# Kernel optimization log

Measured on AMD Instinct MI355X. Metric: run time of the kernel, lower is better.

Reference implementation:

```python
import jax, jax.numpy as jnp
import numpy as np


def _make_coord(n):
    # grid-center coords in (-1, 1), matching make_coord in the torch code
    return -1.0 + 1.0 / n + (2.0 / n) * jnp.arange(n, dtype=jnp.float32)


def _mlp(inp, W1, b1, W2, b2, W3, b3):
    h = jax.nn.relu(inp @ W1 + b1)
    h = jax.nn.relu(h @ W2 + b2)
    return h @ W3 + b3


def setup_inputs() -> dict:
    key = jax.random.key(0)
    ks = jax.random.split(key, 4)
    dim = 64
    x = jax.random.normal(ks[0], (4, dim, 64, 64), dtype=jnp.float32)
    W1 = jax.random.normal(ks[1], (dim + 2, 256), dtype=jnp.float32) * 0.05
    W2 = jax.random.normal(ks[2], (256, 256), dtype=jnp.float32) * 0.05
    W3 = jax.random.normal(ks[3], (256, dim), dtype=jnp.float32) * 0.05
    return {
        "x": x,
        "W1": W1, "b1": jnp.zeros((256,), jnp.float32),
        "W2": W2, "b2": jnp.zeros((256,), jnp.float32),
        "W3": W3, "b3": jnp.zeros((dim,), jnp.float32),
        "h_out": 256, "w_out": 256,
    }


def reference(x, W1, b1, W2, b2, W3, b3, h_out, w_out):
    B, C, H, W = x.shape
    # query coords on the output grid (same for every batch element)
    gy, gx = jnp.meshgrid(_make_coord(h_out), _make_coord(w_out), indexing="ij")
    cy = gy.reshape(-1)  # [Q], coord channel 0 (height)
    cx = gx.reshape(-1)  # [Q], coord channel 1 (width)
    rx = 1.0 / H  # = 2 / H / 2
    ry = 1.0 / W
    eps_shift = 1e-6
    lim = 1.0 - 1e-6
    fy = _make_coord(H)  # feat_coord values along height
    fx = _make_coord(W)

    preds = []
    areas = []
    for vx in (-1.0, 1.0):
        for vy in (-1.0, 1.0):
            sy = jnp.clip(cy + vx * rx + eps_shift, -lim, lim)
            sx = jnp.clip(cx + vy * ry + eps_shift, -lim, lim)
            # grid_sample nearest, align_corners=False: unnormalize then round
            iy = jnp.clip(jnp.round(((sy + 1.0) * H - 1.0) * 0.5), 0, H - 1).astype(jnp.int32)
            ix = jnp.clip(jnp.round(((sx + 1.0) * W - 1.0) * 0.5), 0, W - 1).astype(jnp.int32)
            q_feat = x[:, :, iy, ix].transpose(0, 2, 1)  # [B, Q, C]
            rel_y = (cy - fy[iy]) * H  # [Q]
            rel_x = (cx - fx[ix]) * W
            rel = jnp.stack([rel_y, rel_x], axis=-1)  # [Q, 2]
            inp = jnp.concatenate(
                [q_feat, jnp.broadcast_to(rel, (B,) + rel.shape)], axis=-1
            )  # [B, Q, C+2]
            preds.append(_mlp(inp, W1, b1, W2, b2, W3, b3))  # [B, Q, C]
            areas.append(jnp.abs(rel_y * rel_x) + 1e-9)  # [Q]

    tot_area = areas[0] + areas[1] + areas[2] + areas[3]
    # local_ensemble swap: 0<->3, 1<->2 (opposite-corner area weighting)
    areas = [areas[3], areas[2], areas[1], areas[0]]
    ret = 0.0
    for pred, area in zip(preds, areas):
        ret = ret + pred * (area / tot_area)[None, :, None]
    return ret  # [B, h_out*w_out, C]
```

## Files before the change

kernel.cpp:

```cpp
#include <hip/hip_runtime.h>


typedef __bf16 bf16x8 __attribute__((ext_vector_type(8)));
typedef float  f32x4  __attribute__((ext_vector_type(4)));

#define LDS_SWZ(row, kbyte) ((kbyte) ^ (((row) & 7) << 4))

#define WP1_U 0
#define WP2_U (48 * 512)
#define WP3_U (176 * 512)
#define XT_OFF (1 << 20)

__global__ __launch_bounds__(64) void prep_weights(
    const float* __restrict__ W1, const float* __restrict__ W2,
    const float* __restrict__ W3, ushort* __restrict__ ws)
{
    const int blk = blockIdx.x;
    const int l   = threadIdx.x;
    const float* W; int Kreal, N, ks, nt; size_t off;
    if (blk < 48)       { W = W1; Kreal = 66;  N = 256; ks = blk >> 4;  nt = blk & 15; off = WP1_U + (size_t)blk * 512; }
    else if (blk < 176) { int b2 = blk - 48;  W = W2; Kreal = 256; N = 256; ks = b2 >> 4; nt = b2 & 15; off = WP2_U + (size_t)b2 * 512; }
    else                { int b3 = blk - 176; W = W3; Kreal = 256; N = 64;  ks = b3 >> 2; nt = b3 & 3;  off = WP3_U + (size_t)b3 * 512; }

    const int n = nt * 16 + (l & 15);
    ushort v[8];
    #pragma unroll
    for (int j = 0; j < 8; ++j) {
        const int k = ks * 32 + ((l >> 4) * 8) + j;
        const float f = (k < Kreal) ? W[(size_t)k * N + n] : 0.0f;
        v[j] = __builtin_bit_cast(ushort, (__bf16)f);
    }
    *(uint4*)(ws + off + (size_t)l * 8) = *(const uint4*)v;
}

__global__ __launch_bounds__(256) void prep_xt(const float* __restrict__ x, char* __restrict__ xt)
{
    const int blk = blockIdx.x;
    const int b = blk >> 6, iy = blk & 63;
    const int ix = threadIdx.x & 63, cq = threadIdx.x >> 6;
    ushort v[16];
    #pragma unroll
    for (int j = 0; j < 16; ++j) {
        const int ch = cq * 16 + j;
        const float f = x[(((size_t)b * 64 + ch) * 64 + iy) * 64 + ix];
        v[j] = __builtin_bit_cast(ushort, (__bf16)f);
    }
    char* dst = xt + ((size_t)((b * 4096 + iy * 64 + ix)) * 128) + cq * 32;
    *(uint4*)dst        = *(const uint4*)(v);
    *(uint4*)(dst + 16) = *(const uint4*)(v + 8);
}

__device__ inline void store_hidden(char* __restrict__ dst, const f32x4 (&acc)[4][4],
                                    int lane, int nbase_t)
{
    const int lrow = lane & 15;
    const int lk   = lane >> 4;
    #pragma unroll
    for (int nt = 0; nt < 4; ++nt) {
        const int n  = (nbase_t + nt) * 16 + lrow;
        const int kbyte = 2 * n;
        #pragma unroll
        for (int mt = 0; mt < 4; ++mt) {
            #pragma unroll
            for (int r = 0; r < 4; ++r) {
                const int row = mt * 16 + lk * 4 + r;
                const float v = fmaxf(acc[mt][nt][r], 0.0f);
                *(ushort*)(dst + row * 512 + LDS_SWZ(row, kbyte)) = __builtin_bit_cast(ushort, (__bf16)v);
            }
        }
    }
}

__global__ __launch_bounds__(256, 3) void liif_mfma6_kernel(
    const char* __restrict__ xt,
    const float* __restrict__ b1f, const float* __restrict__ b2f, const float* __restrict__ b3f,
    const ushort* __restrict__ ws, float* __restrict__ out)
{
    __shared__ char bufH[32 * 1024];
    __shared__ float s_w[4][16];

    const int tid  = threadIdx.x;
    const int lane = tid & 63;
    const int wv   = tid >> 6;
    const int lrow = lane & 15;
    const int lk   = lane >> 4;
    const int nbase_t = wv * 4;

    const int bid0 = blockIdx.x;
    const int b    = (bid0 & 7) >> 1;
    const int qidx = (bid0 >> 3) * 2 + (bid0 & 1);
    const int q0   = qidx << 4;

    int   pix_off[4];
    float rely[4], relx[4];
    {
        const int q  = q0 + lrow;
        const int yq = q >> 8, xq = q & 255;
        const float cy  = -1.0f + (2.0f * yq + 1.0f) / 256.0f;
        const float cx  = -1.0f + (2.0f * xq + 1.0f) / 256.0f;
        const float lim = 1.0f - 1e-6f;
        float area[4];
        #pragma unroll
        for (int c = 0; c < 4; ++c) {
            const float vx = (c & 2) ? 1.0f : -1.0f;
            const float vy = (c & 1) ? 1.0f : -1.0f;
            float sy = cy + vx * (1.0f / 64.0f) + 1e-6f;
            float sx = cx + vy * (1.0f / 64.0f) + 1e-6f;
            sy = fminf(fmaxf(sy, -lim), lim);
            sx = fminf(fmaxf(sx, -lim), lim);
            int iyv = (int)rintf(((sy + 1.0f) * 64.0f - 1.0f) * 0.5f);
            int ixv = (int)rintf(((sx + 1.0f) * 64.0f - 1.0f) * 0.5f);
            iyv = min(max(iyv, 0), 63);
            ixv = min(max(ixv, 0), 63);
            const float fy = -1.0f + (2.0f * iyv + 1.0f) / 64.0f;
            const float fx = -1.0f + (2.0f * ixv + 1.0f) / 64.0f;
            rely[c] = (cy - fy) * 64.0f;
            relx[c] = (cx - fx) * 64.0f;
            pix_off[c] = (b * 4096 + iyv * 64 + ixv) * 128;
            area[c] = fabsf(rely[c] * relx[c]) + 1e-9f;
        }
        if (tid < 16) {
            const float tot = area[0] + area[1] + area[2] + area[3];
            #pragma unroll
            for (int c = 0; c < 4; ++c) s_w[c][lrow] = area[3 - c] / tot;
        }
    }

    f32x4 acc[4][4];

    {
        #pragma unroll
        for (int nt = 0; nt < 4; ++nt) {
            const float bs = b1f[(nbase_t + nt) * 16 + lrow];
            #pragma unroll
            for (int mt = 0; mt < 4; ++mt) acc[mt][nt] = (f32x4){bs, bs, bs, bs};
        }
        const ushort* wpl = ws + WP1_U + ((size_t)nbase_t << 9) + (lane << 3);
        #pragma unroll 1
        for (int ks = 0; ks < 2; ++ks) {
            bf16x8 bb[4];
            #pragma unroll
            for (int nt = 0; nt < 4; ++nt)
                bb[nt] = *(const bf16x8*)(wpl + ((size_t)(ks * 16 + nt) << 9));
            #pragma unroll
            for (int mt = 0; mt < 4; ++mt) {
                const bf16x8 a = *(const bf16x8*)(xt + pix_off[mt] + ks * 64 + lk * 16);
                __builtin_amdgcn_s_setprio(1);
                #pragma unroll
                for (int nt = 0; nt < 4; ++nt)
                    acc[mt][nt] = __builtin_amdgcn_mfma_f32_16x16x32_bf16(a, bb[nt], acc[mt][nt], 0, 0, 0);
                __builtin_amdgcn_s_setprio(0);
            }
        }
        {
            bf16x8 bb[4];
            #pragma unroll
            for (int nt = 0; nt < 4; ++nt)
                bb[nt] = *(const bf16x8*)(wpl + ((size_t)(32 + nt) << 9));
            #pragma unroll
            for (int mt = 0; mt < 4; ++mt) {
                bf16x8 a = (bf16x8){0, 0, 0, 0, 0, 0, 0, 0};
                if (lk == 0) { a[0] = (__bf16)rely[mt]; a[1] = (__bf16)relx[mt]; }
                __builtin_amdgcn_s_setprio(1);
                #pragma unroll
                for (int nt = 0; nt < 4; ++nt)
                    acc[mt][nt] = __builtin_amdgcn_mfma_f32_16x16x32_bf16(a, bb[nt], acc[mt][nt], 0, 0, 0);
                __builtin_amdgcn_s_setprio(0);
            }
        }
    }
    store_hidden(bufH, acc, lane, nbase_t);
    __syncthreads();

    {
        #pragma unroll
        for (int nt = 0; nt < 4; ++nt) {
            const float bs = b2f[(nbase_t + nt) * 16 + lrow];
            #pragma unroll
            for (int mt = 0; mt < 4; ++mt) acc[mt][nt] = (f32x4){bs, bs, bs, bs};
        }
        const ushort* wpl = ws + WP2_U + ((size_t)nbase_t << 9) + (lane << 3);
        #pragma unroll 1
        for (int ks = 0; ks < 8; ++ks) {
            bf16x8 bb[4];
            #pragma unroll
            for (int nt = 0; nt < 4; ++nt)
                bb[nt] = *(const bf16x8*)(wpl + ((size_t)(ks * 16 + nt) << 9));
            #pragma unroll
            for (int mt = 0; mt < 4; ++mt) {
                const int row   = mt * 16 + lrow;
                const int kbyte = ks * 64 + lk * 16;
                const bf16x8 a = *(const bf16x8*)(bufH + row * 512 + LDS_SWZ(row, kbyte));
                __builtin_amdgcn_s_setprio(1);
                #pragma unroll
                for (int nt = 0; nt < 4; ++nt)
                    acc[mt][nt] = __builtin_amdgcn_mfma_f32_16x16x32_bf16(a, bb[nt], acc[mt][nt], 0, 0, 0);
                __builtin_amdgcn_s_setprio(0);
            }
        }
    }
    __syncthreads();
    store_hidden(bufH, acc, lane, nbase_t);
    __syncthreads();

    {
        const int nt3 = wv;
        const float bs = b3f[nt3 * 16 + lrow];
        f32x4 acc3[4];
        #pragma unroll
        for (int mt = 0; mt < 4; ++mt) acc3[mt] = (f32x4){bs, bs, bs, bs};

        const ushort* wp3 = ws + WP3_U + (lane << 3);
        #pragma unroll 1
        for (int ks = 0; ks < 8; ++ks) {
            const bf16x8 bb = *(const bf16x8*)(wp3 + ((size_t)(ks * 4 + nt3) << 9));
            #pragma unroll
            for (int mt = 0; mt < 4; ++mt) {
                const int row   = mt * 16 + lrow;
                const int kbyte = ks * 64 + lk * 16;
                const bf16x8 a = *(const bf16x8*)(bufH + row * 512 + LDS_SWZ(row, kbyte));
                __builtin_amdgcn_s_setprio(1);
                acc3[mt] = __builtin_amdgcn_mfma_f32_16x16x32_bf16(a, bb, acc3[mt], 0, 0, 0);
                __builtin_amdgcn_s_setprio(0);
            }
        }
        __syncthreads();
        #pragma unroll
        for (int mt = 0; mt < 4; ++mt) {
            #pragma unroll
            for (int r = 0; r < 4; ++r) {
                const int row = mt * 16 + lk * 4 + r;
                const float wgt = s_w[row >> 4][row & 15];
                const int cb = (nt3 * 16 + lrow) * 4;
                *(float*)(bufH + row * 256 + LDS_SWZ(row, cb)) = acc3[mt][r] * wgt;
            }
        }
    }
    __syncthreads();

    {
        const int q  = tid >> 4;
        const int ch = (tid & 15) * 4;
        f32x4 sum = (f32x4){0.f, 0.f, 0.f, 0.f};
        #pragma unroll
        for (int c = 0; c < 4; ++c) {
            const int row = c * 16 + q;
            const f32x4 v = *(const f32x4*)(bufH + row * 256 + LDS_SWZ(row, ch * 4));
            sum += v;
        }
        *(f32x4*)(out + ((size_t)b * 65536 + q0 + q) * 64 + ch) = sum;
    }
}

extern "C" void kernel_launch(void* const* d_in, const int* in_sizes, int n_in,
                              void* d_out, int out_size, void* d_ws, size_t ws_size,
                              hipStream_t stream) {
    const float* x  = (const float*)d_in[0];
    const float* W1 = (const float*)d_in[1];
    const float* b1 = (const float*)d_in[2];
    const float* W2 = (const float*)d_in[3];
    const float* b2 = (const float*)d_in[4];
    const float* W3 = (const float*)d_in[5];
    const float* b3 = (const float*)d_in[6];
    float* out = (float*)d_out;
    ushort* wp = (ushort*)d_ws;
    char* xt   = (char*)d_ws + XT_OFF;

    prep_weights<<<208, 64, 0, stream>>>(W1, W2, W3, wp);
    prep_xt<<<256, 256, 0, stream>>>(x, xt);
    liif_mfma6_kernel<<<16384, 256, 0, stream>>>(xt, b1, b2, b3, wp, out);
}
```

Measured before the change: 260.1 us.

## Transpose MFMA operand roles so hidden stores pack into vector LDS writes

Weights become the A operand and activations the B operand in every MFMA layer, so each lane's accumulator holds four consecutive output features for one row. The hidden-state store can then pack four bf16 values into one 8-byte LDS write instead of four scalar 2-byte writes, and the final weighted output store becomes one 16-byte write. Bias loads also become vectorised. The aim is to cut LDS store instruction count and bank traffic between layers, at the cost of relying on the prepacked weight layout fitting the transposed operand convention.

Measured after the change: 235.1 us. -9.6%, faster.

```diff
diff --git a/kernel.cpp b/kernel.cpp
--- a/kernel.cpp
+++ b/kernel.cpp
@@ -3,6 +3,7 @@
 
 typedef __bf16 bf16x8 __attribute__((ext_vector_type(8)));
 typedef float  f32x4  __attribute__((ext_vector_type(4)));
+typedef unsigned int u32x2 __attribute__((ext_vector_type(2)));
 
 #define LDS_SWZ(row, kbyte) ((kbyte) ^ (((row) & 7) << 4))
 
@@ -50,28 +51,66 @@
     *(uint4*)(dst + 16) = *(const uint4*)(v + 8);
 }
 
-__device__ inline void store_hidden(char* __restrict__ dst, const f32x4 (&acc)[4][4],
-                                    int lane, int nbase_t)
+__device__ inline unsigned pk2(float a, float b) {
+    return (unsigned)__builtin_bit_cast(ushort, (__bf16)a)
+         | ((unsigned)__builtin_bit_cast(ushort, (__bf16)b) << 16);
+}
+
+template<int KSTEPS>
+__device__ inline void compute_layer_T(const char* __restrict__ src,
+                                       const ushort* __restrict__ wp,
+                                       const float* __restrict__ bias,
+                                       int lane, int wtile4, f32x4 (&acc)[4][4])
 {
     const int lrow = lane & 15;
     const int lk   = lane >> 4;
     #pragma unroll
+    for (int mt = 0; mt < 4; ++mt) {
+        const f32x4 bs = *(const f32x4*)(bias + (wtile4 + mt) * 16 + lk * 4);
+        #pragma unroll
+        for (int nt = 0; nt < 4; ++nt) acc[mt][nt] = bs;
+    }
+    const ushort* wpl = wp + ((size_t)wtile4 << 9) + (lane << 3);
+    #pragma unroll 1
+    for (int ks = 0; ks < KSTEPS; ++ks) {
+        bf16x8 wa[4];
+        #pragma unroll
+        for (int mt = 0; mt < 4; ++mt)
+            wa[mt] = *(const bf16x8*)(wpl + ((size_t)(ks * 16 + mt) << 9));
+        #pragma unroll
+        for (int nt = 0; nt < 4; ++nt) {
+            const int row   = nt * 16 + lrow;
+            const int kbyte = ks * 64 + lk * 16;
+            const bf16x8 hb = *(const bf16x8*)(src + row * 512 + LDS_SWZ(row, kbyte));
+            __builtin_amdgcn_s_setprio(1);
+            #pragma unroll
+            for (int mt = 0; mt < 4; ++mt)
+                acc[mt][nt] = __builtin_amdgcn_mfma_f32_16x16x32_bf16(wa[mt], hb, acc[mt][nt], 0, 0, 0);
+            __builtin_amdgcn_s_setprio(0);
+        }
+    }
+}
+
+__device__ inline void store_hidden_T(char* __restrict__ dst, const f32x4 (&acc)[4][4],
+                                      int lane, int wtile4)
+{
+    const int lrow = lane & 15;
+    const int lk   = lane >> 4;
+    #pragma unroll
     for (int nt = 0; nt < 4; ++nt) {
-        const int n  = (nbase_t + nt) * 16 + lrow;
-        const int kbyte = 2 * n;
+        const int row = nt * 16 + lrow;
         #pragma unroll
         for (int mt = 0; mt < 4; ++mt) {
-            #pragma unroll
-            for (int r = 0; r < 4; ++r) {
-                const int row = mt * 16 + lk * 4 + r;
-                const float v = fmaxf(acc[mt][nt][r], 0.0f);
-                *(ushort*)(dst + row * 512 + LDS_SWZ(row, kbyte)) = __builtin_bit_cast(ushort, (__bf16)v);
-            }
-        }
-    }
-}
-
-__global__ __launch_bounds__(256, 3) void liif_mfma6_kernel(
+            const int nb = ((wtile4 + mt) * 16 + lk * 4) * 2;
+            u32x2 p;
+            p[0] = pk2(fmaxf(acc[mt][nt][0], 0.0f), fmaxf(acc[mt][nt][1], 0.0f));
+            p[1] = pk2(fmaxf(acc[mt][nt][2], 0.0f), fmaxf(acc[mt][nt][3], 0.0f));
+            *(u32x2*)(dst + row * 512 + LDS_SWZ(row, nb)) = p;
+        }
+    }
+}
+
+__global__ __launch_bounds__(256, 3) void liif_mfma8_kernel(
     const char* __restrict__ xt,
     const float* __restrict__ b1f, const float* __restrict__ b2f, const float* __restrict__ b3f,
     const ushort* __restrict__ ws, float* __restrict__ out)
@@ -84,7 +123,7 @@
     const int wv   = tid >> 6;
     const int lrow = lane & 15;
     const int lk   = lane >> 4;
-    const int nbase_t = wv * 4;
+    const int wtile4 = wv * 4;
 
     const int bid0 = blockIdx.x;
     const int b    = (bid0 & 7) >> 1;
@@ -130,110 +169,81 @@
 
     {
         #pragma unroll
-        for (int nt = 0; nt < 4; ++nt) {
-            const float bs = b1f[(nbase_t + nt) * 16 + lrow];
-            #pragma unroll
-            for (int mt = 0; mt < 4; ++mt) acc[mt][nt] = (f32x4){bs, bs, bs, bs};
-        }
-        const ushort* wpl = ws + WP1_U + ((size_t)nbase_t << 9) + (lane << 3);
+        for (int mt = 0; mt < 4; ++mt) {
+            const f32x4 bs = *(const f32x4*)(b1f + (wtile4 + mt) * 16 + lk * 4);
+            #pragma unroll
+            for (int nt = 0; nt < 4; ++nt) acc[mt][nt] = bs;
+        }
+        const ushort* wpl = ws + WP1_U + ((size_t)wtile4 << 9) + (lane << 3);
         #pragma unroll 1
         for (int ks = 0; ks < 2; ++ks) {
-            bf16x8 bb[4];
-            #pragma unroll
-            for (int nt = 0; nt < 4; ++nt)
-                bb[nt] = *(const bf16x8*)(wpl + ((size_t)(ks * 16 + nt) << 9));
-            #pragma unroll
-            for (int mt = 0; mt < 4; ++mt) {
-                const bf16x8 a = *(const bf16x8*)(xt + pix_off[mt] + ks * 64 + lk * 16);
+            bf16x8 wa[4];
+            #pragma unroll
+            for (int mt = 0; mt < 4; ++mt)
+                wa[mt] = *(const bf16x8*)(wpl + ((size_t)(ks * 16 + mt) << 9));
+            #pragma unroll
+            for (int nt = 0; nt < 4; ++nt) {
+                const bf16x8 hb = *(const bf16x8*)(xt + pix_off[nt] + ks * 64 + lk * 16);
                 __builtin_amdgcn_s_setprio(1);
                 #pragma unroll
-                for (int nt = 0; nt < 4; ++nt)
-                    acc[mt][nt] = __builtin_amdgcn_mfma_f32_16x16x32_bf16(a, bb[nt], acc[mt][nt], 0, 0, 0);
+                for (int mt = 0; mt < 4; ++mt)
+                    acc[mt][nt] = __builtin_amdgcn_mfma_f32_16x16x32_bf16(wa[mt], hb, acc[mt][nt], 0, 0, 0);
                 __builtin_amdgcn_s_setprio(0);
             }
         }
         {
-            bf16x8 bb[4];
-            #pragma unroll
-            for (int nt = 0; nt < 4; ++nt)
-                bb[nt] = *(const bf16x8*)(wpl + ((size_t)(32 + nt) << 9));
-            #pragma unroll
-            for (int mt = 0; mt < 4; ++mt) {
-                bf16x8 a = (bf16x8){0, 0, 0, 0, 0, 0, 0, 0};
-                if (lk == 0) { a[0] = (__bf16)rely[mt]; a[1] = (__bf16)relx[mt]; }
+            bf16x8 wa[4];
+            #pragma unroll
+            for (int mt = 0; mt < 4; ++mt)
+                wa[mt] = *(const bf16x8*)(wpl + ((size_t)(32 + mt) << 9));
+            #pragma unroll
+            for (int nt = 0; nt < 4; ++nt) {
+                bf16x8 hb = (bf16x8){0, 0, 0, 0, 0, 0, 0, 0};
+                if (lk == 0) { hb[0] = (__bf16)rely[nt]; hb[1] = (__bf16)relx[nt]; }
                 __builtin_amdgcn_s_setprio(1);
                 #pragma unroll
-                for (int nt = 0; nt < 4; ++nt)
-                    acc[mt][nt] = __builtin_amdgcn_mfma_f32_16x16x32_bf16(a, bb[nt], acc[mt][nt], 0, 0, 0);
+                for (int mt = 0; mt < 4; ++mt)
+                    acc[mt][nt] = __builtin_amdgcn_mfma_f32_16x16x32_bf16(wa[mt], hb, acc[mt][nt], 0, 0, 0);
                 __builtin_amdgcn_s_setprio(0);
             }
         }
     }
-    store_hidden(bufH, acc, lane, nbase_t);
-    __syncthreads();
-
-    {
-        #pragma unroll
-        for (int nt = 0; nt < 4; ++nt) {
-            const float bs = b2f[(nbase_t + nt) * 16 + lrow];
-            #pragma unroll
-            for (int mt = 0; mt < 4; ++mt) acc[mt][nt] = (f32x4){bs, bs, bs, bs};
-        }
-        const ushort* wpl = ws + WP2_U + ((size_t)nbase_t << 9) + (lane << 3);
+    store_hidden_T(bufH, acc, lane, wtile4);
+    __syncthreads();
+
+    compute_layer_T<8>(bufH, ws + WP2_U, b2f, lane, wtile4, acc);
+    __syncthreads();
+    store_hidden_T(bufH, acc, lane, wtile4);
+    __syncthreads();
+
+    {
+        f32x4 acc3[4];
+        const f32x4 bs3 = *(const f32x4*)(b3f + wv * 16 + lk * 4);
+        #pragma unroll
+        for (int mt = 0; mt < 4; ++mt) acc3[mt] = bs3;
+
+        const ushort* wp3 = ws + WP3_U + (lane << 3);
         #pragma unroll 1
         for (int ks = 0; ks < 8; ++ks) {
-            bf16x8 bb[4];
-            #pragma unroll
-            for (int nt = 0; nt < 4; ++nt)
-                bb[nt] = *(const bf16x8*)(wpl + ((size_t)(ks * 16 + nt) << 9));
+            const bf16x8 wa = *(const bf16x8*)(wp3 + ((size_t)(ks * 4 + wv) << 9));
             #pragma unroll
             for (int mt = 0; mt < 4; ++mt) {
                 const int row   = mt * 16 + lrow;
                 const int kbyte = ks * 64 + lk * 16;
-                const bf16x8 a = *(const bf16x8*)(bufH + row * 512 + LDS_SWZ(row, kbyte));
+                const bf16x8 hb = *(const bf16x8*)(bufH + row * 512 + LDS_SWZ(row, kbyte));
                 __builtin_amdgcn_s_setprio(1);
-                #pragma unroll
-                for (int nt = 0; nt < 4; ++nt)
-                    acc[mt][nt] = __builtin_amdgcn_mfma_f32_16x16x32_bf16(a, bb[nt], acc[mt][nt], 0, 0, 0);
+                acc3[mt] = __builtin_amdgcn_mfma_f32_16x16x32_bf16(wa, hb, acc3[mt], 0, 0, 0);
                 __builtin_amdgcn_s_setprio(0);
             }
         }
-    }
-    __syncthreads();
-    store_hidden(bufH, acc, lane, nbase_t);
-    __syncthreads();
-
-    {
-        const int nt3 = wv;
-        const float bs = b3f[nt3 * 16 + lrow];
-        f32x4 acc3[4];
-        #pragma unroll
-        for (int mt = 0; mt < 4; ++mt) acc3[mt] = (f32x4){bs, bs, bs, bs};
-
-        const ushort* wp3 = ws + WP3_U + (lane << 3);
-        #pragma unroll 1
-        for (int ks = 0; ks < 8; ++ks) {
-            const bf16x8 bb = *(const bf16x8*)(wp3 + ((size_t)(ks * 4 + nt3) << 9));
-            #pragma unroll
-            for (int mt = 0; mt < 4; ++mt) {
-                const int row   = mt * 16 + lrow;
-                const int kbyte = ks * 64 + lk * 16;
-                const bf16x8 a = *(const bf16x8*)(bufH + row * 512 + LDS_SWZ(row, kbyte));
-                __builtin_amdgcn_s_setprio(1);
-                acc3[mt] = __builtin_amdgcn_mfma_f32_16x16x32_bf16(a, bb, acc3[mt], 0, 0, 0);
-                __builtin_amdgcn_s_setprio(0);
-            }
-        }
         __syncthreads();
         #pragma unroll
         for (int mt = 0; mt < 4; ++mt) {
-            #pragma unroll
-            for (int r = 0; r < 4; ++r) {
-                const int row = mt * 16 + lk * 4 + r;
-                const float wgt = s_w[row >> 4][row & 15];
-                const int cb = (nt3 * 16 + lrow) * 4;
-                *(float*)(bufH + row * 256 + LDS_SWZ(row, cb)) = acc3[mt][r] * wgt;
-            }
+            const int row = mt * 16 + lrow;
+            const float wgt = s_w[mt][lrow];
+            const f32x4 v = acc3[mt] * wgt;
+            const int cb = wv * 64 + lk * 16;
+            *(f32x4*)(bufH + row * 256 + LDS_SWZ(row, cb)) = v;
         }
     }
     __syncthreads();
@@ -268,5 +278,5 @@
 
     prep_weights<<<208, 64, 0, stream>>>(W1, W2, W3, wp);
     prep_xt<<<256, 256, 0, stream>>>(x, xt);
-    liif_mfma6_kernel<<<16384, 256, 0, stream>>>(xt, b1, b2, b3, wp, out);
-}
+    liif_mfma8_kernel<<<16384, 256, 0, stream>>>(xt, b1, b2, b3, wp, out);
+}
```
